# Kernel optimization log

Hardware: AMD Instinct MI355X
Metric: run time of the kernel (lower is better)

## Reference

```python
import jax, jax.numpy as jnp
import numpy as np

NUM_FRAMES = 2
EPS = 768.0  # torch code calls nn.LayerNorm(hidden_size, hidden_size): eps == hidden_size (faithful)


def setup_inputs() -> dict:
    key = jax.random.key(0)
    ks = jax.random.split(key, 8)
    B, N, D = 64, 1568, 768  # N = 8 frames * 196 patches
    x = jax.random.normal(ks[0], (B, N, D), dtype=jnp.float32)
    inp = jax.random.normal(ks[1], (B, N + 1, D), dtype=jnp.float32)  # class token + patches
    s = 1.0 / np.sqrt(D)
    ln_w = jnp.ones((D,), jnp.float32)
    ln_b = jnp.zeros((D,), jnp.float32)
    w1 = jax.random.normal(ks[2], (D, D), jnp.float32) * s        # linear[0]: D->D
    w2 = jax.random.normal(ks[3], (D, D // 2), jnp.float32) * s   # linear[1]: D->D/2
    w3 = jax.random.normal(ks[4], (D, D), jnp.float32) * s        # linear2[0]: D->D
    w4 = jax.random.normal(ks[5], (D, 1), jnp.float32) * s        # linear2[1]: D->1
    return {"x": x, "inp": inp, "ln_w": ln_w, "ln_b": ln_b,
            "w1": w1, "w2": w2, "w3": w3, "w4": w4}


def reference(x, inp, ln_w, ln_b, w1, w2, w3, w4):
    B, N, D = x.shape
    T = inp.shape[1] - 1
    cls = inp[:, :1]                                   # [B,1,D]
    h = inp[:, 1:].reshape(B, 8, -1)                   # [B,8,(T/8)*D]
    # segment max over tokens within each of 8 frames
    xm = x.reshape(B, 8, N // 8, D).max(axis=2)        # [B,8,D]
    # LayerNorm with eps=768 (faithful to source)
    mu = xm.mean(axis=-1, keepdims=True)
    var = jnp.mean((xm - mu) ** 2, axis=-1, keepdims=True)
    xn = (xm - mu) / jnp.sqrt(var + EPS) * ln_w + ln_b
    # scorer MLP
    x_m = (xn @ w1) @ w2                               # [B,8,D/2]
    x_a = jnp.broadcast_to(x_m.mean(axis=1, keepdims=True), x_m.shape)
    xc = jnp.concatenate([x_m, x_a], axis=-1)          # [B,8,D]
    s = ((xc @ w3) @ w4)[..., 0]                       # [B,8]
    s_max = s.max(axis=1, keepdims=True)
    s_min = s.min(axis=1, keepdims=True)
    s1 = (s - s_min) / (s_max - s_min)
    _, idx = jax.lax.top_k(s1, NUM_FRAMES)             # [B,2]
    # one-hot @ h == row gather; use direct indexed gather
    sel = jnp.take_along_axis(h, idx[:, :, None], axis=1)  # [B,2,(T/8)*D]
    out = sel.reshape(B, NUM_FRAMES * T // 8, D)
    return jnp.concatenate([cls, out], axis=1)         # [B, 1 + 2*T/8, D]
```

## Files before the change

### kernel.cpp

```cpp
#include <hip/hip_runtime.h>
#include <hip/hip_bf16.h>
#include <math.h>


typedef float f32x4 __attribute__((ext_vector_type(4)));
typedef float f32x2 __attribute__((ext_vector_type(2)));

__global__ __launch_bounds__(256) void k_gemv768(const float* __restrict__ M,
                                                 const float* __restrict__ vec,
                                                 float* __restrict__ outv) {
    const int wave = threadIdx.x >> 6;
    const int lane = threadIdx.x & 63;
    const int row = blockIdx.x * 4 + wave;
    const f32x4* r4 = reinterpret_cast<const f32x4*>(M + (size_t)row * 768);
    const f32x4* v4 = reinterpret_cast<const f32x4*>(vec);
    float s = 0.f;
#pragma unroll
    for (int i = 0; i < 3; ++i) {
        f32x4 a = r4[lane + 64 * i];
        f32x4 b = v4[lane + 64 * i];
        s += a.x * b.x + a.y * b.y + a.z * b.z + a.w * b.w;
    }
#pragma unroll
    for (int off = 32; off; off >>= 1) s += __shfl_down(s, off);
    if (lane == 0) outv[row] = s;
}

__global__ __launch_bounds__(256) void k_gemv384(const float* __restrict__ M,
                                                 const float* __restrict__ vec,
                                                 float* __restrict__ outv) {
    const int wave = threadIdx.x >> 6;
    const int lane = threadIdx.x & 63;
    const int row = blockIdx.x * 4 + wave;
    const f32x2* r2 = reinterpret_cast<const f32x2*>(M + (size_t)row * 384);
    const f32x2* v2 = reinterpret_cast<const f32x2*>(vec);
    float s = 0.f;
#pragma unroll
    for (int i = 0; i < 3; ++i) {
        f32x2 a = r2[lane + 64 * i];
        f32x2 b = v2[lane + 64 * i];
        s += a.x * b.x + a.y * b.y;
    }
#pragma unroll
    for (int off = 32; off; off >>= 1) s += __shfl_down(s, off);
    if (lane == 0) outv[row] = s;
}

__global__ __launch_bounds__(768) void k_max_score(const float* __restrict__ x,
                                                   const float* __restrict__ ln_w,
                                                   const float* __restrict__ ln_b,
                                                   const float* __restrict__ u,
                                                   float* __restrict__ t_out) {
    const int bg = blockIdx.x;
    const int b = bg >> 3;
    const int g = bg & 7;
    const int tid = threadIdx.x;
    const int col = tid % 192;
    const int chunk = tid / 192;

    const float lw = ln_w[tid];
    const float lb = ln_b[tid];
    const float ud = u[tid];

    const f32x4* base = reinterpret_cast<const f32x4*>(
        x + ((size_t)b * 1568 + (size_t)g * 196 + (size_t)chunk * 49) * 768) + col;

    f32x4 mx = {-INFINITY, -INFINITY, -INFINITY, -INFINITY};
#pragma unroll 7
    for (int r = 0; r < 49; ++r) {
        f32x4 vv = __builtin_nontemporal_load(base + (size_t)r * 192);
        mx.x = fmaxf(mx.x, vv.x);
        mx.y = fmaxf(mx.y, vv.y);
        mx.z = fmaxf(mx.z, vv.z);
        mx.w = fmaxf(mx.w, vv.w);
    }

    __shared__ f32x4 sm4[4][192];
    __shared__ float red[12][5];

    sm4[chunk][col] = mx;
    __syncthreads();

    const float* smf = reinterpret_cast<const float*>(sm4);
    const float xmd = fmaxf(fmaxf(smf[0 * 768 + tid], smf[1 * 768 + tid]),
                            fmaxf(smf[2 * 768 + tid], smf[3 * 768 + tid]));

    const float lu = lw * ud;
    float a0 = xmd, a1 = xmd * xmd, a2 = xmd * lu, a3 = lu, a4 = lb * ud;
#pragma unroll
    for (int off = 32; off; off >>= 1) {
        a0 += __shfl_down(a0, off);
        a1 += __shfl_down(a1, off);
        a2 += __shfl_down(a2, off);
        a3 += __shfl_down(a3, off);
        a4 += __shfl_down(a4, off);
    }
    const int wave = tid >> 6;
    if ((tid & 63) == 0) {
        red[wave][0] = a0; red[wave][1] = a1; red[wave][2] = a2;
        red[wave][3] = a3; red[wave][4] = a4;
    }
    __syncthreads();
    if (tid == 0) {
        float S0 = 0.f, S1 = 0.f, S2 = 0.f, S3 = 0.f, S4 = 0.f;
#pragma unroll
        for (int w = 0; w < 12; ++w) {
            S0 += red[w][0]; S1 += red[w][1]; S2 += red[w][2];
            S3 += red[w][3]; S4 += red[w][4];
        }
        const float mu   = S0 * (1.0f / 768.0f);
        const float var  = S1 * (1.0f / 768.0f) - mu * mu;
        const float rstd = 1.0f / sqrtf(var + 768.0f);
        t_out[bg] = rstd * (S2 - mu * S3) + S4;
    }
}

__global__ __launch_bounds__(768) void k_gather(const float* __restrict__ inp,
                                                const float* __restrict__ t,
                                                float* __restrict__ out) {
    const int b = blockIdx.x;
    const int chunk = blockIdx.y;
    const int base = chunk * 50;
    const int nrows = min(50, 393 - base);
    const int tid = threadIdx.x;
    const int col = tid % 192;
    const int rsub = tid / 192;

    __shared__ int sIdx[2];
    if (tid == 0) {
        const float* tb = t + b * 8;
        float best = tb[0];
        int i0 = 0;
#pragma unroll
        for (int gi = 1; gi < 8; ++gi) {
            const float v = tb[gi];
            if (v > best) { best = v; i0 = gi; }
        }
        float best2 = -INFINITY;
        int i1 = 0;
#pragma unroll
        for (int gi = 0; gi < 8; ++gi) {
            if (gi == i0) continue;
            const float v = tb[gi];
            if (v > best2) { best2 = v; i1 = gi; }
        }
        sIdx[0] = i0;
        sIdx[1] = i1;
    }
    __syncthreads();
    const int i0 = sIdx[0], i1 = sIdx[1];

    const f32x4* src_b = reinterpret_cast<const f32x4*>(inp) + (size_t)b * 1569 * 192;
    f32x4* dst_b = reinterpret_cast<f32x4*>(out) + (size_t)b * 393 * 192;

    auto src_of = [&](int it) -> const f32x4* {
        const int row = base + rsub + 4 * it;
        int src_row;
        if (row == 0) {
            src_row = 0;
        } else {
            const int q = row - 1;
            const int gsel = (q < 196) ? i0 : i1;
            const int r = (q < 196) ? q : q - 196;
            src_row = 1 + gsel * 196 + r;
        }
        return src_b + (size_t)src_row * 192 + col;
    };

    const int nit = (nrows - rsub + 3) >> 2;
    f32x4 cur = __builtin_nontemporal_load(src_of(0));
    for (int it = 0; it < nit; ++it) {
        f32x4 nxt;
        if (it + 1 < nit) nxt = __builtin_nontemporal_load(src_of(it + 1));
        const int row = base + rsub + 4 * it;
        __builtin_nontemporal_store(cur, dst_b + (size_t)row * 192 + col);
        cur = nxt;
    }
}

extern "C" void kernel_launch(void* const* d_in, const int* in_sizes, int n_in,
                              void* d_out, int out_size, void* d_ws, size_t ws_size,
                              hipStream_t stream) {
    const float* x    = (const float*)d_in[0];
    const float* inp  = (const float*)d_in[1];
    const float* ln_w = (const float*)d_in[2];
    const float* ln_b = (const float*)d_in[3];
    const float* w1   = (const float*)d_in[4];
    const float* w2   = (const float*)d_in[5];
    const float* w3   = (const float*)d_in[6];
    const float* w4   = (const float*)d_in[7];
    float* out = (float*)d_out;

    float* ws = (float*)d_ws;
    float* v = ws;
    float* p = ws + 768;
    float* u = ws + 1536;
    float* t = ws + 2304;

    k_gemv768<<<dim3( 96), dim3(256), 0, stream>>>(w3, w4, v);
    k_gemv384<<<dim3(192), dim3(256), 0, stream>>>(w2, v, p);
    k_gemv768<<<dim3(192), dim3(256), 0, stream>>>(w1, p, u);
    k_max_score<<<dim3(512), dim3(768), 0, stream>>>(x, ln_w, ln_b, u, t);
    k_gather  <<<dim3(64, 8), dim3(768), 0, stream>>>(inp, t, out);
}
```

Before: 90.50 us.

## Fuse GEMV chain and max-score with gather using device-wide atomic barriers

Merges the three weight GEMV launches into one 64-block kernel that uses global atomic spin barriers between stages. It also fuses the segment-max/score kernel with the row gather: each (batch, frame) block waits on a per-batch counter for all 8 scores, picks the top-2, then copies its own slice of output rows. This removes several kernel launches and the serialization gap before the gather, at the cost of a memset and spin-waits. The spin-waits depend on all 8 blocks of a batch being co-resident, which is a deadlock risk if scheduling does not guarantee it.

```diff
diff --git a/kernel.cpp b/kernel.cpp
--- a/kernel.cpp
+++ b/kernel.cpp
@@ -1,56 +1,94 @@
 #include <hip/hip_runtime.h>
-#include <hip/hip_bf16.h>
 #include <math.h>
 
 
 typedef float f32x4 __attribute__((ext_vector_type(4)));
 typedef float f32x2 __attribute__((ext_vector_type(2)));
 
-__global__ __launch_bounds__(256) void k_gemv768(const float* __restrict__ M,
-                                                 const float* __restrict__ vec,
-                                                 float* __restrict__ outv) {
-    const int wave = threadIdx.x >> 6;
-    const int lane = threadIdx.x & 63;
-    const int row = blockIdx.x * 4 + wave;
-    const f32x4* r4 = reinterpret_cast<const f32x4*>(M + (size_t)row * 768);
-    const f32x4* v4 = reinterpret_cast<const f32x4*>(vec);
-    float s = 0.f;
-#pragma unroll
-    for (int i = 0; i < 3; ++i) {
-        f32x4 a = r4[lane + 64 * i];
-        f32x4 b = v4[lane + 64 * i];
-        s += a.x * b.x + a.y * b.y + a.z * b.z + a.w * b.w;
-    }
-#pragma unroll
-    for (int off = 32; off; off >>= 1) s += __shfl_down(s, off);
-    if (lane == 0) outv[row] = s;
+#define SCOPE_AGENT __HIP_MEMORY_SCOPE_AGENT
+
+__global__ __launch_bounds__(256) void k_gemv_chain(
+    const float* __restrict__ w3, const float* __restrict__ w4,
+    const float* __restrict__ w2, const float* __restrict__ w1,
+    float* __restrict__ v, float* __restrict__ p, float* __restrict__ u,
+    int* __restrict__ bar)
+{
+    const int tid = threadIdx.x;
+    const int gw = blockIdx.x * 4 + (tid >> 6);
+    const int lane = tid & 63;
+
+    {
+        const f32x4* b4 = reinterpret_cast<const f32x4*>(w4);
+        for (int r = gw; r < 384; r += 256) {
+            const f32x4* a4 = reinterpret_cast<const f32x4*>(w3 + (size_t)r * 768);
+            float s = 0.f;
+#pragma unroll
+            for (int i = 0; i < 3; ++i) {
+                f32x4 a = a4[lane + 64 * i];
+                f32x4 b = b4[lane + 64 * i];
+                s += a.x * b.x + a.y * b.y + a.z * b.z + a.w * b.w;
+            }
+#pragma unroll
+            for (int off = 32; off; off >>= 1) s += __shfl_down(s, off);
+            if (lane == 0) v[r] = s;
+        }
+    }
+    __syncthreads();
+    if (tid == 0) {
+        __hip_atomic_fetch_add(&bar[0], 1, __ATOMIC_ACQ_REL, SCOPE_AGENT);
+        while (__hip_atomic_load(&bar[0], __ATOMIC_ACQUIRE, SCOPE_AGENT) < 64)
+            __builtin_amdgcn_s_sleep(1);
+    }
+    __syncthreads();
+
+    {
+        const f32x2* b2 = reinterpret_cast<const f32x2*>(v);
+        for (int r = gw; r < 768; r += 256) {
+            const f32x2* a2 = reinterpret_cast<const f32x2*>(w2 + (size_t)r * 384);
+            float s = 0.f;
+#pragma unroll
+            for (int i = 0; i < 3; ++i) {
+                f32x2 a = a2[lane + 64 * i];
+                f32x2 b = b2[lane + 64 * i];
+                s += a.x * b.x + a.y * b.y;
+            }
+#pragma unroll
+            for (int off = 32; off; off >>= 1) s += __shfl_down(s, off);
+            if (lane == 0) p[r] = s;
+        }
+    }
+    __syncthreads();
+    if (tid == 0) {
+        __hip_atomic_fetch_add(&bar[1], 1, __ATOMIC_ACQ_REL, SCOPE_AGENT);
+        while (__hip_atomic_load(&bar[1], __ATOMIC_ACQUIRE, SCOPE_AGENT) < 64)
+            __builtin_amdgcn_s_sleep(1);
+    }
+    __syncthreads();
+
+    {
+        const f32x4* b4 = reinterpret_cast<const f32x4*>(p);
+        for (int r = gw; r < 768; r += 256) {
+            const f32x4* a4 = reinterpret_cast<const f32x4*>(w1 + (size_t)r * 768);
+            float s = 0.f;
+#pragma unroll
+            for (int i = 0; i < 3; ++i) {
+                f32x4 a = a4[lane + 64 * i];
+                f32x4 b = b4[lane + 64 * i];
+                s += a.x * b.x + a.y * b.y + a.z * b.z + a.w * b.w;
+            }
+#pragma unroll
+            for (int off = 32; off; off >>= 1) s += __shfl_down(s, off);
+            if (lane == 0) u[r] = s;
+        }
+    }
 }
 
-__global__ __launch_bounds__(256) void k_gemv384(const float* __restrict__ M,
-                                                 const float* __restrict__ vec,
-                                                 float* __restrict__ outv) {
-    const int wave = threadIdx.x >> 6;
-    const int lane = threadIdx.x & 63;
-    const int row = blockIdx.x * 4 + wave;
-    const f32x2* r2 = reinterpret_cast<const f32x2*>(M + (size_t)row * 384);
-    const f32x2* v2 = reinterpret_cast<const f32x2*>(vec);
-    float s = 0.f;
-#pragma unroll
-    for (int i = 0; i < 3; ++i) {
-        f32x2 a = r2[lane + 64 * i];
-        f32x2 b = v2[lane + 64 * i];
-        s += a.x * b.x + a.y * b.y;
-    }
-#pragma unroll
-    for (int off = 32; off; off >>= 1) s += __shfl_down(s, off);
-    if (lane == 0) outv[row] = s;
-}
-
-__global__ __launch_bounds__(768) void k_max_score(const float* __restrict__ x,
-                                                   const float* __restrict__ ln_w,
-                                                   const float* __restrict__ ln_b,
-                                                   const float* __restrict__ u,
-                                                   float* __restrict__ t_out) {
+__global__ __launch_bounds__(768, 6) void k_stream_gather(
+    const float* __restrict__ x, const float* __restrict__ inp,
+    const float* __restrict__ ln_w, const float* __restrict__ ln_b,
+    const float* __restrict__ u, float* __restrict__ t,
+    int* __restrict__ done, float* __restrict__ out)
+{
     const int bg = blockIdx.x;
     const int b = bg >> 3;
     const int g = bg & 7;
@@ -77,6 +115,7 @@
 
     __shared__ f32x4 sm4[4][192];
     __shared__ float red[12][5];
+    __shared__ int sIdx[2];
 
     sm4[chunk][col] = mx;
     __syncthreads();
@@ -101,6 +140,7 @@
         red[wave][3] = a3; red[wave][4] = a4;
     }
     __syncthreads();
+
     if (tid == 0) {
         float S0 = 0.f, S1 = 0.f, S2 = 0.f, S3 = 0.f, S4 = 0.f;
 #pragma unroll
@@ -111,38 +151,27 @@
         const float mu   = S0 * (1.0f / 768.0f);
         const float var  = S1 * (1.0f / 768.0f) - mu * mu;
         const float rstd = 1.0f / sqrtf(var + 768.0f);
-        t_out[bg] = rstd * (S2 - mu * S3) + S4;
-    }
-}
-
-__global__ __launch_bounds__(768) void k_gather(const float* __restrict__ inp,
-                                                const float* __restrict__ t,
-                                                float* __restrict__ out) {
-    const int b = blockIdx.x;
-    const int chunk = blockIdx.y;
-    const int base = chunk * 50;
-    const int nrows = min(50, 393 - base);
-    const int tid = threadIdx.x;
-    const int col = tid % 192;
-    const int rsub = tid / 192;
-
-    __shared__ int sIdx[2];
-    if (tid == 0) {
-        const float* tb = t + b * 8;
-        float best = tb[0];
+        t[bg] = rstd * (S2 - mu * S3) + S4;
+
+        __hip_atomic_fetch_add(&done[b], 1, __ATOMIC_ACQ_REL, SCOPE_AGENT);
+        while (__hip_atomic_load(&done[b], __ATOMIC_ACQUIRE, SCOPE_AGENT) < 8)
+            __builtin_amdgcn_s_sleep(1);
+
+        float tv[8];
+#pragma unroll
+        for (int gi = 0; gi < 8; ++gi)
+            tv[gi] = __hip_atomic_load(&t[b * 8 + gi], __ATOMIC_RELAXED, SCOPE_AGENT);
+        float best = tv[0];
         int i0 = 0;
 #pragma unroll
-        for (int gi = 1; gi < 8; ++gi) {
-            const float v = tb[gi];
-            if (v > best) { best = v; i0 = gi; }
-        }
+        for (int gi = 1; gi < 8; ++gi)
+            if (tv[gi] > best) { best = tv[gi]; i0 = gi; }
         float best2 = -INFINITY;
         int i1 = 0;
 #pragma unroll
         for (int gi = 0; gi < 8; ++gi) {
             if (gi == i0) continue;
-            const float v = tb[gi];
-            if (v > best2) { best2 = v; i1 = gi; }
+            if (tv[gi] > best2) { best2 = tv[gi]; i1 = gi; }
         }
         sIdx[0] = i0;
         sIdx[1] = i1;
@@ -150,11 +179,15 @@
     __syncthreads();
     const int i0 = sIdx[0], i1 = sIdx[1];
 
+    const int obase = g * 50;
+    const int nrows = min(50, 393 - obase);
+    const int rsub = tid / 192;
+
     const f32x4* src_b = reinterpret_cast<const f32x4*>(inp) + (size_t)b * 1569 * 192;
     f32x4* dst_b = reinterpret_cast<f32x4*>(out) + (size_t)b * 393 * 192;
 
     auto src_of = [&](int it) -> const f32x4* {
-        const int row = base + rsub + 4 * it;
+        const int row = obase + rsub + 4 * it;
         int src_row;
         if (row == 0) {
             src_row = 0;
@@ -172,7 +205,7 @@
     for (int it = 0; it < nit; ++it) {
         f32x4 nxt;
         if (it + 1 < nit) nxt = __builtin_nontemporal_load(src_of(it + 1));
-        const int row = base + rsub + 4 * it;
+        const int row = obase + rsub + 4 * it;
         __builtin_nontemporal_store(cur, dst_b + (size_t)row * 192 + col);
         cur = nxt;
     }
@@ -196,10 +229,12 @@
     float* p = ws + 768;
     float* u = ws + 1536;
     float* t = ws + 2304;
-
-    k_gemv768<<<dim3( 96), dim3(256), 0, stream>>>(w3, w4, v);
-    k_gemv384<<<dim3(192), dim3(256), 0, stream>>>(w2, v, p);
-    k_gemv768<<<dim3(192), dim3(256), 0, stream>>>(w1, p, u);
-    k_max_score<<<dim3(512), dim3(768), 0, stream>>>(x, ln_w, ln_b, u, t);
-    k_gather  <<<dim3(64, 8), dim3(768), 0, stream>>>(inp, t, out);
+    int* bar  = (int*)(ws + 2816);
+    int* done = bar + 2;
+
+    hipMemsetAsync(bar, 0, 66 * sizeof(int), stream);
+
+    k_gemv_chain<<<dim3(64), dim3(256), 0, stream>>>(w3, w4, w2, w1, v, p, u, bar);
+    k_stream_gather<<<dim3(512), dim3(768), 0, stream>>>(x, inp, ln_w, ln_b, u, t,
+                                                         done, out);
 }
```

After: 131.3 us. +45.1%, slower.
